# Optimization experiments

Hardware: AMD Instinct MI355X
Metric: run time of the kernel (lower is better)

The kernel has to match this reference:

```python
import jax, jax.numpy as jnp
import numpy as np
import math

H = 300
B = 2048
SEG = 48
N = B * SEG

def _gru_direction(x_seq, h0, w_ih, w_hh, b_ih, b_hh, reverse):
    # x_seq: [L, B, H]; h0: [B, H]; w_ih/w_hh: [3H, H]; b_ih/b_hh: [3H]
    xp = jnp.einsum('lbh,gh->lbg', x_seq, w_ih) + b_ih  # precompute input projections [L,B,3H]
    def step(h, xp_t):
        hp = h @ w_hh.T + b_hh
        xr, xz, xn = jnp.split(xp_t, 3, axis=-1)
        hr, hz, hn = jnp.split(hp, 3, axis=-1)
        r = jax.nn.sigmoid(xr + hr)
        z = jax.nn.sigmoid(xz + hz)
        n = jnp.tanh(xn + r * hn)
        h_new = (1.0 - z) * n + z * h
        return h_new, h_new
    _, ys = jax.lax.scan(step, h0, xp, reverse=reverse)
    return ys  # [L, B, H]

def setup_inputs() -> dict:
    key = jax.random.key(0)
    ks = jax.random.split(key, 12)
    bound = 1.0 / math.sqrt(H)
    u = lambda k, shape: jax.random.uniform(k, shape, jnp.float32, -bound, bound)
    x = jax.random.normal(ks[0], (N, H), jnp.float32)
    batch = jnp.repeat(jnp.arange(B, dtype=jnp.int32), SEG)  # sorted segment ids
    return {
        'x': x,
        'batch': batch,
        'num_moles': B,
        'max_len': SEG,
        'bias': u(ks[1], (H,)),
        'w_ih_f': u(ks[2], (3 * H, H)),
        'w_hh_f': u(ks[3], (3 * H, H)),
        'b_ih_f': u(ks[4], (3 * H,)),
        'b_hh_f': u(ks[5], (3 * H,)),
        'w_ih_b': u(ks[6], (3 * H, H)),
        'w_hh_b': u(ks[7], (3 * H, H)),
        'b_ih_b': u(ks[8], (3 * H,)),
        'b_hh_b': u(ks[9], (3 * H,)),
    }

def reference(x, batch, num_moles, max_len, bias, w_ih_f, w_hh_f, b_ih_f, b_hh_f, w_ih_b, w_hh_b, b_ih_b, b_hh_b):
    n, h = x.shape
    message = jax.nn.relu(x + bias)
    counts = jax.ops.segment_sum(jnp.ones_like(batch), batch, num_segments=num_moles)
    offsets = jnp.cumsum(counts) - counts
    pos = jnp.arange(n, dtype=batch.dtype) - offsets[batch]  # position within molecule
    # ragged -> padded pack [B, L, H]
    padded = jnp.zeros((num_moles, max_len, h), x.dtype).at[batch, pos].set(message)
    # initial hidden = per-molecule max over raw x (same h0 for both directions)
    h0 = jax.ops.segment_max(x, batch, num_segments=num_moles)  # [B, H]
    xs = padded.transpose(1, 0, 2)  # [L, B, H]
    yf = _gru_direction(xs, h0, w_ih_f, w_hh_f, b_ih_f, b_hh_f, reverse=False)
    yb = _gru_direction(xs, h0, w_ih_b, w_hh_b, b_ih_b, b_hh_b, reverse=True)
    y = jnp.concatenate([yf, yb], axis=-1).transpose(1, 0, 2)  # [B, L, 2H]
    return y[batch, pos]  # unpad -> [N, 2H]
```

## Files before the change

kernel.cpp:

```cpp
#include <hip/hip_runtime.h>
#include <hip/hip_bf16.h>

#define H    300
#define KP   320
#define BM   2048
#define SEG  48
#define NTOK (BM*SEG)
#define G    900
#define GP   912
#define NT   57
#define GW   1024
#define XPW  912
#define MOLW 16
#define WGT  1024
#define NPAIR (MOLW*150)
#define PIT  3
#define BKX  64

typedef __attribute__((ext_vector_type(8))) short short8;
typedef __attribute__((ext_vector_type(4))) float f32x4;

__device__ __forceinline__ float lo16(unsigned u) { return __uint_as_float(u << 16); }
__device__ __forceinline__ float hi16(unsigned u) { return __uint_as_float(u & 0xffff0000u); }
__device__ __forceinline__ unsigned short bfb(float f) {
    __hip_bfloat16 b = __float2bfloat16(f);
    return *(unsigned short*)&b;
}
__device__ __forceinline__ void gload16(const void* g, void* l) {
    __builtin_amdgcn_global_load_lds((const __attribute__((address_space(1))) unsigned*)g,
                                     (__attribute__((address_space(3))) unsigned*)l, 16, 0, 0);
}

__global__ void prep_weights(const float* wih_f, const float* whh_f, const float* bih_f,
                             const float* wih_b, const float* whh_b, const float* bih_b,
                             __hip_bfloat16* wih, __hip_bfloat16* whh, float* bih) {
    int idx = blockIdx.x * 256 + threadIdx.x;
    const int wih_n = 2 * GW * KP;
    const int whh_n = 2 * GP * KP;
    if (idx < wih_n) {
        int d = idx / (GW * KP);
        int r = (idx / KP) % GW;
        int k = idx % KP;
        const float* src = d ? wih_b : wih_f;
        float v = (r < G && k < H) ? src[r * H + k] : 0.f;
        wih[idx] = __float2bfloat16(v);
        return;
    }
    idx -= wih_n;
    if (idx < whh_n) {
        int d = idx / (GP * KP);
        int r = (idx / KP) % GP;
        int k = idx % KP;
        const float* src = d ? whh_b : whh_f;
        float v = (r < G && k < H) ? src[r * H + k] : 0.f;
        whh[idx] = __float2bfloat16(v);
        return;
    }
    idx -= whh_n;
    if (idx < 2 * GW) {
        int d = idx / GW;
        int r = idx % GW;
        const float* src = d ? bih_b : bih_f;
        bih[idx] = (r < G) ? src[r] : 0.f;
    }
}

__global__ void prep_msg(const float* x, const float* bias, __hip_bfloat16* msg) {
    int idx = blockIdx.x * 256 + threadIdx.x;
    if (idx >= NTOK * KP) return;
    int i = idx / KP, k = idx % KP;
    float v = 0.f;
    if (k < H) {
        v = x[i * H + k] + bias[k];
        v = v > 0.f ? v : 0.f;
    }
    msg[idx] = __float2bfloat16(v);
}

__global__ void h0_kernel(const float* x, float* h0) {
    int m = blockIdx.x;
    for (int c = threadIdx.x; c < H; c += blockDim.x) {
        const float* base = x + (long long)m * SEG * H + c;
        float v = -INFINITY;
        for (int t = 0; t < SEG; t++) v = fmaxf(v, base[t * H]);
        h0[m * H + c] = v;
    }
}

__global__ __launch_bounds__(256) void xp_gemm(const __hip_bfloat16* msg, const __hip_bfloat16* wih,
                                               const float* bih, __hip_bfloat16* xp) {
    int d = blockIdx.z;
    const __hip_bfloat16* A  = msg;
    const __hip_bfloat16* Bw = wih + d * GW * KP;
    const float* bi = bih + d * GW;
    __hip_bfloat16* out = xp + (long long)d * NTOK * XPW;

    __shared__ __hip_bfloat16 sA[128 * BKX];
    __shared__ __hip_bfloat16 sB[128 * BKX];
    const short* sAs = (const short*)sA;
    const short* sBs = (const short*)sB;

    int tid = threadIdx.x;
    int lane = tid & 63, wid = tid >> 6;
    int l15 = lane & 15, quad = lane >> 4;
    int mblk = blockIdx.x * 128, nblk = blockIdx.y * 128;
    int mbase = (wid >> 1) * 64, nbase = (wid & 1) * 64;

    int srow = wid * 32 + (lane >> 3);
    int scc  = (lane & 7) ^ (srow & 7);
    const short* gA0 = (const short*)A  + (long long)(mblk + srow) * KP + scc * 8;
    const short* gB0 = (const short*)Bw + (long long)(nblk + srow) * KP + scc * 8;
    int xsw = (l15 & 7) << 3;

    f32x4 acc[4][4] = {};
    for (int kc = 0; kc < KP / BKX; kc++) {
#pragma unroll
        for (int j = 0; j < 4; j++)
            gload16(gA0 + (long long)j * 8 * KP + kc * BKX, (char*)sA + (wid * 4 + j) * 1024);
#pragma unroll
        for (int j = 0; j < 4; j++)
            gload16(gB0 + (long long)j * 8 * KP + kc * BKX, (char*)sB + (wid * 4 + j) * 1024);
        __syncthreads();

        short8 af[4][2], bf[4][2];
#pragma unroll
        for (int i = 0; i < 4; i++)
#pragma unroll
            for (int kh = 0; kh < 2; kh++)
                af[i][kh] = *(const short8*)(sAs + (mbase + i * 16 + l15) * BKX + ((kh * 32 + quad * 8) ^ xsw));
#pragma unroll
        for (int j = 0; j < 4; j++)
#pragma unroll
            for (int kh = 0; kh < 2; kh++)
                bf[j][kh] = *(const short8*)(sBs + (nbase + j * 16 + l15) * BKX + ((kh * 32 + quad * 8) ^ xsw));
#pragma unroll
        for (int i = 0; i < 4; i++)
#pragma unroll
            for (int j = 0; j < 4; j++) {
                acc[i][j] = __builtin_amdgcn_mfma_f32_16x16x32_bf16(af[i][0], bf[j][0], acc[i][j], 0, 0, 0);
                acc[i][j] = __builtin_amdgcn_mfma_f32_16x16x32_bf16(af[i][1], bf[j][1], acc[i][j], 0, 0, 0);
            }
        __syncthreads();
    }

#pragma unroll
    for (int i = 0; i < 4; i++)
#pragma unroll
        for (int j = 0; j < 4; j++) {
            int col = nblk + nbase + j * 16 + l15;
            if (col < XPW) {
                float bv = bi[col];
#pragma unroll
                for (int r = 0; r < 4; r++) {
                    int row = mblk + mbase + i * 16 + quad * 4 + r;
                    out[(long long)row * XPW + col] = __float2bfloat16(acc[i][j][r] + bv);
                }
            }
        }
}

__global__ __launch_bounds__(WGT, 4) void gru_kernel(const __hip_bfloat16* whh_all, const float* bhh_f,
                                                     const float* bhh_b, const __hip_bfloat16* xp,
                                                     const float* h0, float* out) {
    int grp = blockIdx.x;
    int d   = blockIdx.y;
    const short* Ws = (const short*)(whh_all + d * GP * KP);
    const float* bhh = d ? bhh_b : bhh_f;
    const __hip_bfloat16* xpd = xp + (long long)d * NTOK * XPW;

    int tid = threadIdx.x;
    int lane = tid & 63, wid = tid >> 6;
    int l15 = lane & 15, quad = lane >> 4;

    __shared__ __hip_bfloat16 hB[MOLW * 328];
    __shared__ __hip_bfloat16 hp[MOLW * GP];
    const short* hBs = (const short*)hB;

    int mol0 = grp * MOLW;

    for (int e = tid; e < MOLW * 328; e += WGT) hB[e] = __float2bfloat16(0.f);

    const short* bpp[4];
    float bvw[4];
#pragma unroll
    for (int k = 0; k < 4; k++) {
        int nt = wid + 16 * k;
        int ntc = (nt < NT) ? nt : wid;
        bpp[k] = Ws + (ntc * 16 + l15) * KP;
        int gc = nt * 16 + l15;
        bvw[k] = (nt < NT && gc < G) ? bhh[gc] : 0.f;
    }

    int m_[PIT], c_[PIT], xoff[PIT];
#pragma unroll
    for (int i = 0; i < PIT; i++) {
        int e2 = tid + i * WGT;
        int e2c = (e2 < NPAIR) ? e2 : 0;
        m_[i] = e2c / 150; c_[i] = 2 * (e2c % 150);
        xoff[i] = (mol0 + m_[i]) * SEG * XPW + c_[i];
    }
    __syncthreads();

    float hv0[PIT], hv1[PIT];
#pragma unroll
    for (int i = 0; i < PIT; i++) {
        int e2 = tid + i * WGT;
        if (e2 < NPAIR) {
            float2 hh = *(const float2*)(h0 + (size_t)(mol0 + m_[i]) * H + c_[i]);
            hv0[i] = hh.x; hv1[i] = hh.y;
            unsigned pack = ((unsigned)bfb(hh.y) << 16) | bfb(hh.x);
            *(unsigned*)(&hB[m_[i] * 328 + c_[i]]) = pack;
        }
    }
    __syncthreads();

    unsigned pcr[PIT], pcz[PIT], pcn[PIT];
    {
        int tt0 = d ? (SEG - 1) : 0;
#pragma unroll
        for (int i = 0; i < PIT; i++) {
            if (tid + i * WGT < NPAIR) {
                const __hip_bfloat16* xr = xpd + xoff[i] + tt0 * XPW;
                pcr[i] = *(const unsigned*)(xr);
                pcz[i] = *(const unsigned*)(xr + 300);
                pcn[i] = *(const unsigned*)(xr + 600);
            }
        }
    }

    for (int t = 0; t < SEG; t++) {
        int tt = d ? (SEG - 1 - t) : t;

        f32x4 acc[4] = {};
        short8 bq[3][4];
        short8 aq[2];
#pragma unroll
        for (int k = 0; k < 4; k++) {
            bq[0][k] = *(const short8*)(bpp[k] + 0 * 32 + quad * 8);
            bq[1][k] = *(const short8*)(bpp[k] + 1 * 32 + quad * 8);
            bq[2][k] = *(const short8*)(bpp[k] + 2 * 32 + quad * 8);
        }
        aq[0] = *(const short8*)(hBs + l15 * 328 + 0 * 32 + quad * 8);
        aq[1] = *(const short8*)(hBs + l15 * 328 + 1 * 32 + quad * 8);
#pragma unroll
        for (int kk = 0; kk < 10; kk++) {
#pragma unroll
            for (int k = 0; k < 4; k++)
                acc[k] = __builtin_amdgcn_mfma_f32_16x16x32_bf16(aq[kk & 1], bq[kk % 3][k], acc[k], 0, 0, 0);
            if (kk < 7) {
#pragma unroll
                for (int k = 0; k < 4; k++)
                    bq[kk % 3][k] = *(const short8*)(bpp[k] + (kk + 3) * 32 + quad * 8);
            }
            if (kk < 8)
                aq[kk & 1] = *(const short8*)(hBs + l15 * 328 + (kk + 2) * 32 + quad * 8);
        }

        unsigned pnr[PIT] = {0}, pnz[PIT] = {0}, pnn[PIT] = {0};
        if (t + 1 < SEG) {
            int tn = d ? (SEG - 2 - t) : (t + 1);
#pragma unroll
            for (int i = 0; i < PIT; i++) {
                if (tid + i * WGT < NPAIR) {
                    const __hip_bfloat16* xr = xpd + xoff[i] + tn * XPW;
                    pnr[i] = *(const unsigned*)(xr);
                    pnz[i] = *(const unsigned*)(xr + 300);
                    pnn[i] = *(const unsigned*)(xr + 600);
                }
            }
        }

#pragma unroll
        for (int k = 0; k < 4; k++) {
            int nt = wid + 16 * k;
            if (nt < NT) {
                int gcol = nt * 16 + l15;
#pragma unroll
                for (int r = 0; r < 4; r++)
                    hp[(quad * 4 + r) * GP + gcol] = __float2bfloat16(acc[k][r] + bvw[k]);
            }
        }
        __syncthreads();

#pragma unroll
        for (int i = 0; i < PIT; i++) {
            int e2 = tid + i * WGT;
            if (e2 < NPAIR) {
                int m = m_[i], c = c_[i];
                unsigned hr2 = *(const unsigned*)(&hp[m * GP + c]);
                unsigned hz2 = *(const unsigned*)(&hp[m * GP + c + 300]);
                unsigned hn2 = *(const unsigned*)(&hp[m * GP + c + 600]);

                float xr0 = lo16(pcr[i]), xr1 = hi16(pcr[i]);
                float xz0 = lo16(pcz[i]), xz1 = hi16(pcz[i]);
                float xn0 = lo16(pcn[i]), xn1 = hi16(pcn[i]);
                float hr0 = lo16(hr2),  hr1 = hi16(hr2);
                float hz0 = lo16(hz2),  hz1 = hi16(hz2);
                float hn0 = lo16(hn2),  hn1 = hi16(hn2);

                float rg0 = 1.f / (1.f + __expf(-(xr0 + hr0)));
                float rg1 = 1.f / (1.f + __expf(-(xr1 + hr1)));
                float zg0 = 1.f / (1.f + __expf(-(xz0 + hz0)));
                float zg1 = 1.f / (1.f + __expf(-(xz1 + hz1)));
                float ni0 = xn0 + rg0 * hn0;
                float ni1 = xn1 + rg1 * hn1;
                float ng0 = 1.f - 2.f / (__expf(2.f * ni0) + 1.f);
                float ng1 = 1.f - 2.f / (__expf(2.f * ni1) + 1.f);
                float h0n = (1.f - zg0) * ng0 + zg0 * hv0[i];
                float h1n = (1.f - zg1) * ng1 + zg1 * hv1[i];
                hv0[i] = h0n; hv1[i] = h1n;

                unsigned pack = ((unsigned)bfb(h1n) << 16) | bfb(h0n);
                *(unsigned*)(&hB[m * 328 + c]) = pack;

                long long tok = (long long)(mol0 + m) * SEG + tt;
                *(float2*)(out + tok * 600 + d * 300 + c) = make_float2(h0n, h1n);
            }
        }
#pragma unroll
        for (int i = 0; i < PIT; i++) { pcr[i] = pnr[i]; pcz[i] = pnz[i]; pcn[i] = pnn[i]; }
        __syncthreads();
    }
}

extern "C" void kernel_launch(void* const* d_in, const int* in_sizes, int n_in,
                              void* d_out, int out_size, void* d_ws, size_t ws_size,
                              hipStream_t stream) {
    const float* x     = (const float*)d_in[0];
    const float* bias  = (const float*)d_in[4];
    const float* wih_f = (const float*)d_in[5];
    const float* whh_f = (const float*)d_in[6];
    const float* bih_f = (const float*)d_in[7];
    const float* bhh_f = (const float*)d_in[8];
    const float* wih_b = (const float*)d_in[9];
    const float* whh_b = (const float*)d_in[10];
    const float* bih_b = (const float*)d_in[11];
    const float* bhh_b = (const float*)d_in[12];
    float* out = (float*)d_out;

    char* ws = (char*)d_ws;
    __hip_bfloat16* msg = (__hip_bfloat16*)(ws);
    __hip_bfloat16* wih = (__hip_bfloat16*)(ws + 62914560LL);
    __hip_bfloat16* whh = (__hip_bfloat16*)(ws + 64225280LL);
    float*          bih = (float*)         (ws + 65392640LL);
    float*          h0  = (float*)         (ws + 65400832LL);
    __hip_bfloat16* xp  = (__hip_bfloat16*)(ws + 67858432LL);

    hipLaunchKernelGGL(prep_weights, dim3((2*GW*KP + 2*GP*KP + 2*GW + 255) / 256), dim3(256), 0, stream,
                       wih_f, whh_f, bih_f, wih_b, whh_b, bih_b, wih, whh, bih);
    hipLaunchKernelGGL(prep_msg, dim3((NTOK * KP + 255) / 256), dim3(256), 0, stream, x, bias, msg);
    hipLaunchKernelGGL(h0_kernel, dim3(BM), dim3(256), 0, stream, x, h0);
    hipLaunchKernelGGL(xp_gemm, dim3(NTOK / 128, GW / 128, 2), dim3(256), 0, stream, msg, wih, bih, xp);
    hipLaunchKernelGGL(gru_kernel, dim3(BM / MOLW, 2), dim3(WGT), 0, stream, whh, bhh_f, bhh_b, xp, h0, out);
}
```

Measured before the change: 1.610 ms.

## Interleave GRU gate weights per column tile and stream W_hh through LDS

The W_ih, W_hh and bias rows are permuted so that each 16-column tile holds its r, z and n gate rows next to each other. Each wave can then compute all three gate pre-activations for its own hidden columns and apply the GRU update directly in registers. This removes the hp shared-memory round trip and the cross-thread element-pair mapping. W_hh is now staged chunk-by-chunk into double-buffered 64KB LDS buffers with global_load_lds and an XOR swizzle, instead of each wave reading fragments straight from global memory. The cost is ten extra block-wide barriers per timestep, about 138KB of LDS per block, and reduced per-wave MFMA parallelism, since three waves own two tiles and the rest own one.

After: 1.810 ms. +12.4%, slower.

```diff
diff --git a/kernel.cpp b/kernel.cpp
--- a/kernel.cpp
+++ b/kernel.cpp
@@ -7,21 +7,16 @@
 #define SEG  48
 #define NTOK (BM*SEG)
 #define G    900
-#define GP   912
-#define NT   57
 #define GW   1024
 #define XPW  912
 #define MOLW 16
-#define WGT  1024
-#define NPAIR (MOLW*150)
-#define PIT  3
+#define NCH  10
 #define BKX  64
 
 typedef __attribute__((ext_vector_type(8))) short short8;
 typedef __attribute__((ext_vector_type(4))) float f32x4;
 
-__device__ __forceinline__ float lo16(unsigned u) { return __uint_as_float(u << 16); }
-__device__ __forceinline__ float hi16(unsigned u) { return __uint_as_float(u & 0xffff0000u); }
+__device__ __forceinline__ float us2f(unsigned short u) { return __uint_as_float(((unsigned)u) << 16); }
 __device__ __forceinline__ unsigned short bfb(float f) {
     __hip_bfloat16 b = __float2bfloat16(f);
     return *(unsigned short*)&b;
@@ -35,33 +30,38 @@
                              const float* wih_b, const float* whh_b, const float* bih_b,
                              __hip_bfloat16* wih, __hip_bfloat16* whh, float* bih) {
     int idx = blockIdx.x * 256 + threadIdx.x;
-    const int wih_n = 2 * GW * KP;
-    const int whh_n = 2 * GP * KP;
-    if (idx < wih_n) {
+    const int wn = 2 * GW * KP;
+    if (idx < wn) {
         int d = idx / (GW * KP);
-        int r = (idx / KP) % GW;
+        int R = (idx / KP) % GW;
         int k = idx % KP;
+        int ct = R / 48, rem = R % 48, g = rem / 16, i = rem % 16;
+        int col = ct * 16 + i;
         const float* src = d ? wih_b : wih_f;
-        float v = (r < G && k < H) ? src[r * H + k] : 0.f;
+        float v = (R < 912 && col < H && k < H) ? src[(g * H + col) * H + k] : 0.f;
         wih[idx] = __float2bfloat16(v);
         return;
     }
-    idx -= wih_n;
-    if (idx < whh_n) {
-        int d = idx / (GP * KP);
-        int r = (idx / KP) % GP;
+    idx -= wn;
+    if (idx < wn) {
+        int d = idx / (GW * KP);
+        int R = (idx / KP) % GW;
         int k = idx % KP;
+        int ct = R / 48, rem = R % 48, g = rem / 16, i = rem % 16;
+        int col = ct * 16 + i;
         const float* src = d ? whh_b : whh_f;
-        float v = (r < G && k < H) ? src[r * H + k] : 0.f;
+        float v = (R < 912 && col < H && k < H) ? src[(g * H + col) * H + k] : 0.f;
         whh[idx] = __float2bfloat16(v);
         return;
     }
-    idx -= whh_n;
+    idx -= wn;
     if (idx < 2 * GW) {
         int d = idx / GW;
-        int r = idx % GW;
+        int R = idx % GW;
+        int ct = R / 48, rem = R % 48, g = rem / 16, i = rem % 16;
+        int col = ct * 16 + i;
         const float* src = d ? bih_b : bih_f;
-        bih[idx] = (r < G) ? src[r] : 0.f;
+        bih[idx] = (R < 912 && col < H) ? src[g * H + col] : 0.f;
     }
 }
 
@@ -159,166 +159,138 @@
         }
 }
 
-__global__ __launch_bounds__(WGT, 4) void gru_kernel(const __hip_bfloat16* whh_all, const float* bhh_f,
-                                                     const float* bhh_b, const __hip_bfloat16* xp,
-                                                     const float* h0, float* out) {
+__global__ __launch_bounds__(1024) void gru_kernel(const __hip_bfloat16* whh_all, const float* bhh_f,
+                                                   const float* bhh_b, const __hip_bfloat16* xp,
+                                                   const float* h0, float* out) {
     int grp = blockIdx.x;
     int d   = blockIdx.y;
-    const short* Ws = (const short*)(whh_all + d * GP * KP);
+    const char* whhd = (const char*)(whh_all + (long long)d * GW * KP);
     const float* bhh = d ? bhh_b : bhh_f;
     const __hip_bfloat16* xpd = xp + (long long)d * NTOK * XPW;
 
     int tid = threadIdx.x;
     int lane = tid & 63, wid = tid >> 6;
     int l15 = lane & 15, quad = lane >> 4;
+    int xor3 = (l15 & 3) ^ ((l15 >> 2) & 3);
 
     __shared__ __hip_bfloat16 hB[MOLW * 328];
-    __shared__ __hip_bfloat16 hp[MOLW * GP];
-    const short* hBs = (const short*)hB;
+    __shared__ char bufA[65536];
+    __shared__ char bufB[65536];
 
     int mol0 = grp * MOLW;
 
-    for (int e = tid; e < MOLW * 328; e += WGT) hB[e] = __float2bfloat16(0.f);
-
-    const short* bpp[4];
-    float bvw[4];
-#pragma unroll
-    for (int k = 0; k < 4; k++) {
-        int nt = wid + 16 * k;
-        int ntc = (nt < NT) ? nt : wid;
-        bpp[k] = Ws + (ntc * 16 + l15) * KP;
-        int gc = nt * 16 + l15;
-        bvw[k] = (nt < NT && gc < G) ? bhh[gc] : 0.f;
-    }
-
-    int m_[PIT], c_[PIT], xoff[PIT];
-#pragma unroll
-    for (int i = 0; i < PIT; i++) {
-        int e2 = tid + i * WGT;
-        int e2c = (e2 < NPAIR) ? e2 : 0;
-        m_[i] = e2c / 150; c_[i] = 2 * (e2c % 150);
-        xoff[i] = (mol0 + m_[i]) * SEG * XPW + c_[i];
-    }
+    const char* dmasrc[4];
+#pragma unroll
+    for (int j = 0; j < 4; j++) {
+        int R = (wid * 4 + j) * 16 + (lane >> 2);
+        int s = lane & 3;
+        int sw = s ^ (R & 3) ^ ((R >> 2) & 3);
+        dmasrc[j] = whhd + R * (KP * 2) + sw * 16;
+    }
+
+    int nct = (wid < 3) ? 2 : 1;
+
+    for (int e = tid; e < MOLW * 328; e += 1024) hB[e] = __float2bfloat16(0.f);
     __syncthreads();
 
-    float hv0[PIT], hv1[PIT];
-#pragma unroll
-    for (int i = 0; i < PIT; i++) {
-        int e2 = tid + i * WGT;
-        if (e2 < NPAIR) {
-            float2 hh = *(const float2*)(h0 + (size_t)(mol0 + m_[i]) * H + c_[i]);
-            hv0[i] = hh.x; hv1[i] = hh.y;
-            unsigned pack = ((unsigned)bfb(hh.y) << 16) | bfb(hh.x);
-            *(unsigned*)(&hB[m_[i] * 328 + c_[i]]) = pack;
+    float bvv[2][3];
+    f32x4 hreg[2];
+#pragma unroll
+    for (int cc = 0; cc < 2; cc++) {
+        if (cc < nct) {
+            int ct = cc ? 16 + wid : wid;
+            int col = ct * 16 + l15;
+            bool cv = col < H;
+#pragma unroll
+            for (int g = 0; g < 3; g++)
+                bvv[cc][g] = cv ? bhh[g * H + col] : 0.f;
+#pragma unroll
+            for (int r = 0; r < 4; r++) {
+                float hv = cv ? h0[(size_t)(mol0 + quad * 4 + r) * H + col] : 0.f;
+                hreg[cc][r] = hv;
+                if (cv) hB[(quad * 4 + r) * 328 + col] = __float2bfloat16(hv);
+            }
         }
     }
+
+#pragma unroll
+    for (int j = 0; j < 4; j++)
+        gload16(dmasrc[j], bufA + (wid * 4 + j) * 1024);
     __syncthreads();
-
-    unsigned pcr[PIT], pcz[PIT], pcn[PIT];
-    {
-        int tt0 = d ? (SEG - 1) : 0;
-#pragma unroll
-        for (int i = 0; i < PIT; i++) {
-            if (tid + i * WGT < NPAIR) {
-                const __hip_bfloat16* xr = xpd + xoff[i] + tt0 * XPW;
-                pcr[i] = *(const unsigned*)(xr);
-                pcz[i] = *(const unsigned*)(xr + 300);
-                pcn[i] = *(const unsigned*)(xr + 600);
-            }
-        }
-    }
 
     for (int t = 0; t < SEG; t++) {
         int tt = d ? (SEG - 1 - t) : t;
 
-        f32x4 acc[4] = {};
-        short8 bq[3][4];
-        short8 aq[2];
-#pragma unroll
-        for (int k = 0; k < 4; k++) {
-            bq[0][k] = *(const short8*)(bpp[k] + 0 * 32 + quad * 8);
-            bq[1][k] = *(const short8*)(bpp[k] + 1 * 32 + quad * 8);
-            bq[2][k] = *(const short8*)(bpp[k] + 2 * 32 + quad * 8);
+        f32x4 acc[2][3] = {};
+        unsigned short xv[2][3][4];
+
+        auto phase = [&](int c, const char* curb, char* nxtb) {
+            int nk = (c + 1) % NCH;
+#pragma unroll
+            for (int j = 0; j < 4; j++)
+                gload16(dmasrc[j] + nk * 64, nxtb + (wid * 4 + j) * 1024);
+            if (c == 8) {
+#pragma unroll
+                for (int cc = 0; cc < 2; cc++)
+                    if (cc < nct) {
+                        int ct = cc ? 16 + wid : wid;
+#pragma unroll
+                        for (int r = 0; r < 4; r++) {
+                            long long tok = (long long)(mol0 + quad * 4 + r) * SEG + tt;
+                            const unsigned short* xrow = (const unsigned short*)(xpd + tok * XPW + ct * 48 + l15);
+#pragma unroll
+                            for (int g = 0; g < 3; g++)
+                                xv[cc][g][r] = xrow[g * 16];
+                        }
+                    }
+            }
+            short8 aq = *(const short8*)((const char*)hB + l15 * 656 + c * 64 + quad * 16);
+#pragma unroll
+            for (int cc = 0; cc < 2; cc++)
+                if (cc < nct) {
+                    int ct = cc ? 16 + wid : wid;
+#pragma unroll
+                    for (int g = 0; g < 3; g++) {
+                        short8 bq = *(const short8*)(curb + (ct * 48 + g * 16 + l15) * 64 + ((quad ^ xor3) << 4));
+                        acc[cc][g] = __builtin_amdgcn_mfma_f32_16x16x32_bf16(aq, bq, acc[cc][g], 0, 0, 0);
+                    }
+                }
+            __syncthreads();
+        };
+
+#pragma unroll
+        for (int c2 = 0; c2 < 5; c2++) {
+            phase(2 * c2,     bufA, bufB);
+            phase(2 * c2 + 1, bufB, bufA);
         }
-        aq[0] = *(const short8*)(hBs + l15 * 328 + 0 * 32 + quad * 8);
-        aq[1] = *(const short8*)(hBs + l15 * 328 + 1 * 32 + quad * 8);
-#pragma unroll
-        for (int kk = 0; kk < 10; kk++) {
-#pragma unroll
-            for (int k = 0; k < 4; k++)
-                acc[k] = __builtin_amdgcn_mfma_f32_16x16x32_bf16(aq[kk & 1], bq[kk % 3][k], acc[k], 0, 0, 0);
-            if (kk < 7) {
-#pragma unroll
-                for (int k = 0; k < 4; k++)
-                    bq[kk % 3][k] = *(const short8*)(bpp[k] + (kk + 3) * 32 + quad * 8);
-            }
-            if (kk < 8)
-                aq[kk & 1] = *(const short8*)(hBs + l15 * 328 + (kk + 2) * 32 + quad * 8);
-        }
-
-        unsigned pnr[PIT] = {0}, pnz[PIT] = {0}, pnn[PIT] = {0};
-        if (t + 1 < SEG) {
-            int tn = d ? (SEG - 2 - t) : (t + 1);
-#pragma unroll
-            for (int i = 0; i < PIT; i++) {
-                if (tid + i * WGT < NPAIR) {
-                    const __hip_bfloat16* xr = xpd + xoff[i] + tn * XPW;
-                    pnr[i] = *(const unsigned*)(xr);
-                    pnz[i] = *(const unsigned*)(xr + 300);
-                    pnn[i] = *(const unsigned*)(xr + 600);
+
+#pragma unroll
+        for (int cc = 0; cc < 2; cc++)
+            if (cc < nct) {
+                int ct = cc ? 16 + wid : wid;
+                int col = ct * 16 + l15;
+                bool cv = col < H;
+#pragma unroll
+                for (int r = 0; r < 4; r++) {
+                    float hr = acc[cc][0][r] + bvv[cc][0];
+                    float hz = acc[cc][1][r] + bvv[cc][1];
+                    float hn = acc[cc][2][r] + bvv[cc][2];
+                    float xr = us2f(xv[cc][0][r]);
+                    float xz = us2f(xv[cc][1][r]);
+                    float xn = us2f(xv[cc][2][r]);
+                    float rg = 1.f / (1.f + __expf(-(xr + hr)));
+                    float zg = 1.f / (1.f + __expf(-(xz + hz)));
+                    float ni = xn + rg * hn;
+                    float ng = 1.f - 2.f / (__expf(2.f * ni) + 1.f);
+                    float hnew = (1.f - zg) * ng + zg * hreg[cc][r];
+                    hreg[cc][r] = hnew;
+                    if (cv) {
+                        hB[(quad * 4 + r) * 328 + col] = __float2bfloat16(hnew);
+                        long long tok = (long long)(mol0 + quad * 4 + r) * SEG + tt;
+                        out[tok * 600 + d * 300 + col] = hnew;
+                    }
                 }
             }
-        }
-
-#pragma unroll
-        for (int k = 0; k < 4; k++) {
-            int nt = wid + 16 * k;
-            if (nt < NT) {
-                int gcol = nt * 16 + l15;
-#pragma unroll
-                for (int r = 0; r < 4; r++)
-                    hp[(quad * 4 + r) * GP + gcol] = __float2bfloat16(acc[k][r] + bvw[k]);
-            }
-        }
-        __syncthreads();
-
-#pragma unroll
-        for (int i = 0; i < PIT; i++) {
-            int e2 = tid + i * WGT;
-            if (e2 < NPAIR) {
-                int m = m_[i], c = c_[i];
-                unsigned hr2 = *(const unsigned*)(&hp[m * GP + c]);
-                unsigned hz2 = *(const unsigned*)(&hp[m * GP + c + 300]);
-                unsigned hn2 = *(const unsigned*)(&hp[m * GP + c + 600]);
-
-                float xr0 = lo16(pcr[i]), xr1 = hi16(pcr[i]);
-                float xz0 = lo16(pcz[i]), xz1 = hi16(pcz[i]);
-                float xn0 = lo16(pcn[i]), xn1 = hi16(pcn[i]);
-                float hr0 = lo16(hr2),  hr1 = hi16(hr2);
-                float hz0 = lo16(hz2),  hz1 = hi16(hz2);
-                float hn0 = lo16(hn2),  hn1 = hi16(hn2);
-
-                float rg0 = 1.f / (1.f + __expf(-(xr0 + hr0)));
-                float rg1 = 1.f / (1.f + __expf(-(xr1 + hr1)));
-                float zg0 = 1.f / (1.f + __expf(-(xz0 + hz0)));
-                float zg1 = 1.f / (1.f + __expf(-(xz1 + hz1)));
-                float ni0 = xn0 + rg0 * hn0;
-                float ni1 = xn1 + rg1 * hn1;
-                float ng0 = 1.f - 2.f / (__expf(2.f * ni0) + 1.f);
-                float ng1 = 1.f - 2.f / (__expf(2.f * ni1) + 1.f);
-                float h0n = (1.f - zg0) * ng0 + zg0 * hv0[i];
-                float h1n = (1.f - zg1) * ng1 + zg1 * hv1[i];
-                hv0[i] = h0n; hv1[i] = h1n;
-
-                unsigned pack = ((unsigned)bfb(h1n) << 16) | bfb(h0n);
-                *(unsigned*)(&hB[m * 328 + c]) = pack;
-
-                long long tok = (long long)(mol0 + m) * SEG + tt;
-                *(float2*)(out + tok * 600 + d * 300 + c) = make_float2(h0n, h1n);
-            }
-        }
-#pragma unroll
-        for (int i = 0; i < PIT; i++) { pcr[i] = pnr[i]; pcz[i] = pnz[i]; pcn[i] = pnn[i]; }
         __syncthreads();
     }
 }
@@ -342,14 +314,14 @@
     __hip_bfloat16* msg = (__hip_bfloat16*)(ws);
     __hip_bfloat16* wih = (__hip_bfloat16*)(ws + 62914560LL);
     __hip_bfloat16* whh = (__hip_bfloat16*)(ws + 64225280LL);
-    float*          bih = (float*)         (ws + 65392640LL);
-    float*          h0  = (float*)         (ws + 65400832LL);
-    __hip_bfloat16* xp  = (__hip_bfloat16*)(ws + 67858432LL);
-
-    hipLaunchKernelGGL(prep_weights, dim3((2*GW*KP + 2*GP*KP + 2*GW + 255) / 256), dim3(256), 0, stream,
+    float*          bih = (float*)         (ws + 65536000LL);
+    float*          h0  = (float*)         (ws + 65544192LL);
+    __hip_bfloat16* xp  = (__hip_bfloat16*)(ws + 68001792LL);
+
+    hipLaunchKernelGGL(prep_weights, dim3((2*GW*KP + 2*GW*KP + 2*GW + 255) / 256), dim3(256), 0, stream,
                        wih_f, whh_f, bih_f, wih_b, whh_b, bih_b, wih, whh, bih);
     hipLaunchKernelGGL(prep_msg, dim3((NTOK * KP + 255) / 256), dim3(256), 0, stream, x, bias, msg);
     hipLaunchKernelGGL(h0_kernel, dim3(BM), dim3(256), 0, stream, x, h0);
     hipLaunchKernelGGL(xp_gemm, dim3(NTOK / 128, GW / 128, 2), dim3(256), 0, stream, msg, wih, bih, xp);
-    hipLaunchKernelGGL(gru_kernel, dim3(BM / MOLW, 2), dim3(WGT), 0, stream, whh, bhh_f, bhh_b, xp, h0, out);
-}
+    hipLaunchKernelGGL(gru_kernel, dim3(BM / MOLW, 2), dim3(1024), 0, stream, whh, bhh_f, bhh_b, xp, h0, out);
+}
```
